# Optimization experiments

Hardware: AMD Instinct MI355X
Metric: run time of the kernel (lower is better)

## Reference

```python
import jax, jax.numpy as jnp
import numpy as np

DIM = 384; KEY_DIM = 32; HEADS = 8; ATTN_RATIO = 4; RES = 14
D = ATTN_RATIO * KEY_DIM          # 128
DH = D * HEADS                    # 1024
QK = HEADS * KEY_DIM              # 256
B = 64
EPS = 1e-5
SCALE = KEY_DIM ** -0.5


def _bn(x, p):
    # inference-mode BatchNorm; p = [gamma, beta, mean, var] each [C]; channel axis = 1
    g, b, m, v = p
    shp = (1, -1) + (1,) * (x.ndim - 2)
    return (x - m.reshape(shp)) * jax.lax.rsqrt(v.reshape(shp) + EPS) * g.reshape(shp) + b.reshape(shp)


def _bn_params(k, c):
    k1, k2, k3, k4 = jax.random.split(k, 4)
    gamma = 1.0 + 0.1 * jax.random.normal(k1, (c,), dtype=jnp.float32)
    beta = 0.02 * jax.random.normal(k2, (c,), dtype=jnp.float32)
    mean = 0.1 * jax.random.normal(k3, (c,), dtype=jnp.float32)
    var = jax.random.uniform(k4, (c,), dtype=jnp.float32) + 0.5
    return jnp.stack([gamma, beta, mean, var])


def setup_inputs() -> dict:
    key = jax.random.key(0)
    ks = jax.random.split(key, 24)
    def rn(i, shape, s=0.05):
        return s * jax.random.normal(ks[i], shape, dtype=jnp.float32)
    # relative-position bias index table: offset (|dy|,|dx|) -> dy*RES+dx
    coords = np.stack(np.meshgrid(np.arange(RES), np.arange(RES), indexing='ij'), -1).reshape(-1, 2)
    off = np.abs(coords[:, None, :] - coords[None, :, :])  # [N,N,2]
    bias_idxs = jnp.asarray(off[..., 0] * RES + off[..., 1], dtype=jnp.int32)  # [N,N]
    return {
        'x': jax.random.normal(ks[0], (B, DIM, RES, RES), dtype=jnp.float32),
        'wq': rn(1, (QK, DIM)), 'bq': rn(2, (QK,)), 'bnq': _bn_params(ks[3], QK),
        'wk': rn(4, (QK, DIM)), 'bk': rn(5, (QK,)), 'bnk': _bn_params(ks[6], QK),
        'wv': rn(7, (DH, DIM)), 'bv': rn(8, (DH,)), 'bnv': _bn_params(ks[9], DH),
        'wvl': rn(10, (DH, 1, 3, 3)), 'bvl': rn(11, (DH,)), 'bnvl': _bn_params(ks[12], DH),
        'th1w': rn(13, (HEADS, HEADS), 0.2), 'th1b': rn(14, (HEADS,)),
        'th2w': rn(15, (HEADS, HEADS), 0.2), 'th2b': rn(16, (HEADS,)),
        'wp': rn(17, (DIM, DH)), 'bp': rn(18, (DIM,)), 'bnp': _bn_params(ks[19], DIM),
        'ab': rn(20, (HEADS, RES * RES), 0.1),
        'bias_idxs': bias_idxs,
    }


def reference(x, wq, bq, bnq, wk, bk, bnk, wv, bv, bnv, wvl, bvl, bnvl,
              th1w, th1b, th2w, th2b, wp, bp, bnp, ab, bias_idxs):
    Bn, C, H, W = x.shape
    N = H * W
    xf = x.reshape(Bn, C, N)
    # 1x1 conv + BN branches (channel GEMMs)
    q = _bn(jnp.einsum('oc,bcn->bon', wq, xf) + bq[None, :, None], bnq)
    k = _bn(jnp.einsum('oc,bcn->bon', wk, xf) + bk[None, :, None], bnk)
    v = _bn(jnp.einsum('oc,bcn->bon', wv, xf) + bv[None, :, None], bnv)  # [B,DH,N]
    # local value path: 3x3 depthwise conv + BN
    v_img = v.reshape(Bn, DH, H, W)
    v_local = jax.lax.conv_general_dilated(
        v_img, wvl, window_strides=(1, 1), padding='SAME',
        feature_group_count=DH, dimension_numbers=('NCHW', 'OIHW', 'NCHW'))
    v_local = _bn(v_local + bvl[None, :, None, None], bnvl)
    # attention
    qh = q.reshape(Bn, HEADS, KEY_DIM, N).transpose(0, 1, 3, 2)  # b h n d
    kh = k.reshape(Bn, HEADS, KEY_DIM, N)                        # b h d m
    vh = v.reshape(Bn, HEADS, D, N).transpose(0, 1, 3, 2)        # b h m e
    attn = jnp.einsum('bhnd,bhdm->bhnm', qh, kh) * SCALE
    attn = attn + ab[:, bias_idxs][None]                         # [1,H,N,N] positional bias
    attn = jnp.einsum('oh,bhnm->bonm', th1w, attn) + th1b[None, :, None, None]
    attn = jax.nn.softmax(attn, axis=-1)
    attn = jnp.einsum('oh,bhnm->bonm', th2w, attn) + th2b[None, :, None, None]
    out = jnp.einsum('bhnm,bhme->bhne', attn, vh)                # b h n e
    out = out.transpose(0, 1, 3, 2).reshape(Bn, DH, H, W) + v_local
    # proj: ReLU -> 1x1 conv -> BN
    out = jax.nn.relu(out)
    out = jnp.einsum('oc,bchw->bohw', wp, out) + bp[None, :, None, None]
    return _bn(out, bnp)
```

## Files before the change

kernel.cpp:

```cpp
#include <hip/hip_runtime.h>

#define B_     64
#define DIM_   384
#define RES_   14
#define N_     196
#define HEADS_ 8
#define KD_    32
#define D_     128
#define DH_    1024
#define QK_    256
#define CH_    1536
#define EPS_   1e-5f
#define SCALE_ 0.17677669529663687f

typedef unsigned short u16;
typedef unsigned int u32;
typedef short v8s __attribute__((ext_vector_type(8)));
typedef float v4f __attribute__((ext_vector_type(4)));
typedef u16  v4u __attribute__((ext_vector_type(4)));

static __device__ __forceinline__ u16 f2bf(float f) {
    unsigned int u = __builtin_bit_cast(unsigned int, f);
    u = (u + 0x7fffu + ((u >> 16) & 1u)) >> 16;
    return (u16)u;
}
static __device__ __forceinline__ float bf2f(u16 u) {
    unsigned int x = ((unsigned int)u) << 16;
    return __builtin_bit_cast(float, x);
}
static __device__ __forceinline__ u16 f2h(float f) {
    _Float16 h = (_Float16)f;
    return __builtin_bit_cast(u16, h);
}
static __device__ __forceinline__ float h2f(u16 u) {
    return (float)__builtin_bit_cast(_Float16, u);
}

#define WBI_OFF  0u
#define WPI_OFF  589824u
#define QI_OFF   983040u
#define KI_OFF   5177344u
#define VI_OFF   9371648u
#define PBI_OFF  24051712u
#define VLOC_U16 53411840u
#define TAIL_OFF 79101952u
#define TB_OFF   98770944u
#define ABT_OFF  98782720u
#define BIASE_OFF 98785920u

template<int KSTEPS>
static __device__ __forceinline__ void gemm_direct(
    const u16* __restrict__ Ag, const u16* __restrict__ Bg,
    v4f acc[4][4], int tid)
{
    const int lane = tid & 63, w = tid >> 6;
    const int wm = (w & 1) * 64, wn = (w >> 1) * 64;
    const int quad = lane >> 4, l16 = lane & 15;
    const u16* pa = Ag + quad * 1024 + (wm + l16) * 8;
    const u16* pb = Bg + quad * 1024 + (wn + l16) * 8;
    v8s a[2][4], b[2][4];
    #pragma unroll
    for (int i = 0; i < 4; i++) {
        a[0][i] = *(const v8s*)(pa + i * 128);
        b[0][i] = *(const v8s*)(pb + i * 128);
    }
    #pragma unroll
    for (int ks = 0; ks < KSTEPS; ks++) {
        const int cur = ks & 1, nxt = cur ^ 1;
        if (ks + 1 < KSTEPS) {
            const u16* qa = pa + (size_t)(ks + 1) * 4096;
            const u16* qb = pb + (size_t)(ks + 1) * 4096;
            #pragma unroll
            for (int i = 0; i < 4; i++) {
                a[nxt][i] = *(const v8s*)(qa + i * 128);
                b[nxt][i] = *(const v8s*)(qb + i * 128);
            }
        }
        #pragma unroll
        for (int i = 0; i < 4; i++)
            #pragma unroll
            for (int j = 0; j < 4; j++)
                acc[i][j] = __builtin_amdgcn_mfma_f32_16x16x32_bf16(a[cur][i], b[cur][j], acc[i][j], 0, 0, 0);
    }
}

__global__ __launch_bounds__(256) void k_castW(
    const float* __restrict__ wq, const float* __restrict__ wk,
    const float* __restrict__ wv, const float* __restrict__ wp,
    const float* __restrict__ ab,
    const float* __restrict__ th1w, const float* __restrict__ th1b,
    const float* __restrict__ bq, const float* __restrict__ bnq,
    const float* __restrict__ bk, const float* __restrict__ bnk,
    const float* __restrict__ bv, const float* __restrict__ bnv,
    const float* __restrict__ bp, const float* __restrict__ bnp,
    const float* __restrict__ bvl, const float* __restrict__ bnvl,
    u16* __restrict__ WbI, u16* __restrict__ WpI,
    float* __restrict__ abT1, float* __restrict__ TB)
{
    int i = blockIdx.x * 256 + threadIdx.x;
    if (i < 589824) {
        int mt = i / 49152, rem = i % 49152;
        int ks = rem >> 12, r2 = rem & 4095;
        int q = r2 >> 10, row = (r2 >> 3) & 127, e = r2 & 7;
        int c = mt * 128 + row, k = ks * 32 + q * 8 + e;
        float v = (c < 256) ? wq[c * 384 + k]
                : (c < 512) ? wk[(c - 256) * 384 + k]
                            : wv[(size_t)(c - 512) * 384 + k];
        WbI[i] = f2bf(v);
    } else if (i < 983040) {
        int j = i - 589824;
        int mt = j >> 17, rem = j & 131071;
        int ks = rem >> 12, r2 = rem & 4095;
        int q = r2 >> 10, row = (r2 >> 3) & 127, e = r2 & 7;
        int p = mt * 128 + row, k = ks * 32 + q * 8 + e;
        WpI[j] = f2bf(wp[(size_t)p * 1024 + k]);
    } else if (i < 984608) {
        int j = i - 983040;
        int idx = j >> 3, o = j & 7;
        float a = th1b[o];
        #pragma unroll
        for (int h = 0; h < 8; h++) a += th1w[o * 8 + h] * ab[h * N_ + idx];
        abT1[j] = a;
    } else if (i < 987552) {
        int j = i - 984608;
        if (j < 256) {
            int c = j;
            float s = bnq[c] * rsqrtf(bnq[768 + c] + EPS_);
            float t = (bq[c] - bnq[512 + c]) * s + bnq[256 + c];
            TB[c] = s * SCALE_; TB[256 + c] = t * SCALE_;
        } else if (j < 512) {
            int c = j - 256;
            float s = bnk[c] * rsqrtf(bnk[768 + c] + EPS_);
            float t = (bk[c] - bnk[512 + c]) * s + bnk[256 + c];
            TB[512 + c] = s; TB[768 + c] = t;
        } else if (j < 1536) {
            int c = j - 512;
            float s = bnv[c] * rsqrtf(bnv[3072 + c] + EPS_);
            float t = (bv[c] - bnv[2048 + c]) * s + bnv[1024 + c];
            TB[1024 + c] = s; TB[2048 + c] = t;
        } else if (j < 1920) {
            int c = j - 1536;
            float s = bnp[c] * rsqrtf(bnp[1152 + c] + EPS_);
            float t = (bp[c] - bnp[768 + c]) * s + bnp[384 + c];
            TB[3072 + c] = s; TB[3456 + c] = t;
        } else {
            int c = j - 1920;
            float s = bnvl[c] * rsqrtf(bnvl[3072 + c] + EPS_);
            float t = (bvl[c] - bnvl[2048 + c]) * s + bnvl[1024 + c];
            TB[3840 + c] = s; TB[4864 + c] = t;
        }
    }
}

__global__ __launch_bounds__(256) void k_bias(
    const float* __restrict__ abT1, const int* __restrict__ bidx,
    float* __restrict__ biasE)
{
    int i = blockIdx.x * 256 + threadIdx.x;
    if (i >= N_ * 8 * N_) return;
    int m = i % N_;
    int t = i / N_;
    int o = t & 7;
    int n = t >> 3;
    biasE[i] = abT1[bidx[n * N_ + m] * 8 + o] - 5.f;
}

__global__ __launch_bounds__(256) void k_castX(
    const float* __restrict__ x, u16* __restrict__ xI)
{
    __shared__ float T[64][65];
    const int tid = threadIdx.x;
    const int n0 = blockIdx.x * 64;
    const int k0 = blockIdx.y * 64;
    const int b  = blockIdx.z;
    const int c = tid & 63, r4 = tid >> 6;
    #pragma unroll
    for (int i = 0; i < 16; i++) {
        int kr = i * 4 + r4;
        int gn = n0 + c;
        T[kr][c] = (gn < N_) ? x[((size_t)b * DIM_ + k0 + kr) * N_ + gn] : 0.f;
    }
    __syncthreads();
    #pragma unroll
    for (int it = 0; it < 16; it++) {
        int j = it * 256 + tid;
        int kk = j & 63, nn = j >> 6;
        int k = k0 + kk, n = n0 + nn;
        xI[(size_t)b * 98304 + (n >> 7) * 49152 + (k >> 5) * 4096
           + ((k >> 3) & 3) * 1024 + (n & 127) * 8 + (k & 7)] = f2bf(T[kk][nn]);
    }
}

__global__ __launch_bounds__(256) void k_qkv(
    const u16* __restrict__ WbI, const u16* __restrict__ xI,
    const float* __restrict__ TB,
    u16* __restrict__ qI, u16* __restrict__ kI, u16* __restrict__ vI)
{
    const int tid = threadIdx.x;
    const int L = blockIdx.x + 2 * (blockIdx.y + 12 * blockIdx.z);
    const int idx = L >> 3;
    const int b  = (L & 7) * 8 + idx / 24;
    const int r  = idx % 24;
    const int mt = r >> 1, nt = r & 1;
    v4f acc[4][4] = {};
    gemm_direct<12>(WbI + (size_t)mt * 49152,
                    xI + ((size_t)b * 2 + nt) * 49152, acc, tid);

    const int lane = tid & 63, w = tid >> 6;
    const int wm = (w & 1) * 64, wn = (w >> 1) * 64;
    const int quad = lane >> 4, l16 = lane & 15;
    #pragma unroll
    for (int i = 0; i < 4; i++) {
        #pragma unroll
        for (int j = 0; j < 4; j++) {
            int gc = mt * 128 + wm + i * 16 + quad * 4;
            int n  = nt * 128 + wn + j * 16 + l16;
            v4f v = acc[i][j];
            if (gc < 256) {
                v4f s = *(const v4f*)&TB[gc];
                v4f t = *(const v4f*)&TB[256 + gc];
                v4u u;
                #pragma unroll
                for (int r2 = 0; r2 < 4; r2++) u[r2] = f2bf(v[r2] * s[r2] + t[r2]);
                *(v4u*)&qI[((size_t)(b * 8 + (gc >> 5)) * 256 + n) * 32 + (gc & 31)] = u;
            } else if (gc < 512) {
                int c = gc - 256;
                v4f s = *(const v4f*)&TB[512 + c];
                v4f t = *(const v4f*)&TB[768 + c];
                v4u u;
                #pragma unroll
                for (int r2 = 0; r2 < 4; r2++) u[r2] = f2bf(v[r2] * s[r2] + t[r2]);
                *(v4u*)&kI[((size_t)(b * 8 + (c >> 5)) * 256 + n) * 32 + (c & 31)] = u;
            } else {
                int c = gc - 512;
                if (n < 224) {
                    int o = c >> 7, e = c & 127;
                    u16* base = vI + ((size_t)(b * 8 + o) * 7 + (n >> 5)) * 4096
                                + ((n >> 3) & 3) * 1024 + (n & 7);
                    #pragma unroll
                    for (int r2 = 0; r2 < 4; r2++) {
                        u16 outv = 0;
                        if (n < N_) outv = f2bf(v[r2] * TB[1024 + c + r2] + TB[2048 + c + r2]);
                        base[(e + r2) * 8] = outv;
                    }
                }
            }
        }
    }
}

__global__ __launch_bounds__(256) void k_dwconv(
    const u16* __restrict__ vI, const float* __restrict__ wvl,
    const float* __restrict__ TB, u16* __restrict__ vlocI)
{
    __shared__ u16 V[64 * 230];
    const int tid = threadIdx.x;
    const int sub = blockIdx.x;
    const int b   = blockIdx.y;
    const int o   = sub >> 1;
    const int e0  = (sub & 1) * 64;
    const u16* img = vI + (size_t)(b * 8 + o) * 28672;

    {
        const int quad = tid >> 6, l = tid & 63;
        #pragma unroll
        for (int i = 0; i < 7; i++) {
            v8s u = *(const v8s*)&img[i * 4096 + quad * 1024 + (e0 + l) * 8];
            const u32* ui = (const u32*)&u;
            int m0 = i * 32 + quad * 8;
            u32* dst = (u32*)&V[l * 230 + m0];
            #pragma unroll
            for (int c = 0; c < 4; c++) dst[c] = ui[c];
        }
    }
    __syncthreads();

    const int e = tid & 63, j = tid >> 6;
    const int cg = sub * 64 + e;
    const int y0 = j * 4;
    const int ny = (j == 3) ? 2 : 4;
    float wgt[9];
    #pragma unroll
    for (int k = 0; k < 9; k++) wgt[k] = wvl[cg * 9 + k];
    const float sc = TB[3840 + cg], sh = TB[4864 + cg];
    u32 po[4][7];

    for (int yi = 0; yi < ny; yi++) {
        int y = y0 + yi;
        float a[3][16];
        #pragma unroll
        for (int dy = 0; dy < 3; dy++) {
            int yy = y + dy - 1;
            a[dy][0] = 0.f; a[dy][15] = 0.f;
            if (yy < 0 || yy > 13) {
                #pragma unroll
                for (int x = 1; x < 15; x++) a[dy][x] = 0.f;
            } else {
                const u16* rp = &V[e * 230 + yy * 14];
                #pragma unroll
                for (int c4 = 0; c4 < 7; c4++) {
                    u32 u = *(const u32*)&rp[c4 * 2];
                    a[dy][1 + 2 * c4] = bf2f((u16)(u & 0xffffu));
                    a[dy][2 + 2 * c4] = bf2f((u16)(u >> 16));
                }
            }
        }
        #pragma unroll
        for (int xp = 0; xp < 7; xp++) {
            u32 pk = 0;
            #pragma unroll
            for (int half = 0; half < 2; half++) {
                int x = 2 * xp + half;
                float s = 0.f;
                #pragma unroll
                for (int dy = 0; dy < 3; dy++)
                    #pragma unroll
                    for (int kx = 0; kx < 3; kx++)
                        s += wgt[dy * 3 + kx] * a[dy][x + kx];
                u16 bv = f2bf(s * sc + sh);
                pk |= ((u32)bv) << (16 * half);
            }
            po[yi][xp] = pk;
        }
    }
    __syncthreads();

    for (int yi = 0; yi < ny; yi++) {
        u32* dst = (u32*)&V[e * 196 + (y0 + yi) * 14];
        #pragma unroll
        for (int xp = 0; xp < 7; xp++) dst[xp] = po[yi][xp];
    }
    __syncthreads();

    for (int it = 0; it < 7; it++) {
        int idx = it * 256 + tid;
        if (idx < 1568) {
            int g = idx / 196, n = idx - g * 196;
            v4u lo, hi;
            #pragma unroll
            for (int r = 0; r < 4; r++) lo[r] = V[(g * 8 + r) * 196 + n];
            #pragma unroll
            for (int r = 0; r < 4; r++) hi[r] = V[(g * 8 + 4 + r) * 196 + n];
            u16* dst = vlocI + ((size_t)(b * 2 + (n >> 7)) * 32 + sub * 2 + (g >> 2)) * 4096
                     + (g & 3) * 1024 + (n & 127) * 8;
            *(v4u*)dst = lo;
            *(v4u*)(dst + 4) = hi;
        }
    }
}

__global__ __launch_bounds__(256) void k_attn_av(
    const u16* __restrict__ qI, const u16* __restrict__ kI,
    const u16* __restrict__ vI,
    const float* __restrict__ th1w,
    const float* __restrict__ th2w, const float* __restrict__ th2b,
    const float* __restrict__ biasE,
    const u16* __restrict__ vlocI, u16* __restrict__ aoI)
{
    __shared__ u16 Sl[8 * 8 * 228];
    __shared__ float red[64][4];
    __shared__ float invS[64];
    const int tid = threadIdx.x;
    const int w = tid >> 6, lane = tid & 63;
    const int quad = lane >> 4, l16 = lane & 15;
    const int L = blockIdx.x + 25 * blockIdx.y;
    const int idx = L >> 3;
    const int b  = (L & 7) * 8 + idx / 25;
    const int qt = idx % 25;
    const int n0 = qt * 8;

    #pragma unroll
    for (int hh = 0; hh < 2; hh++) {
        int h = w * 2 + hh;
        const u16* qb = qI + (size_t)(b * 8 + h) * 8192;
        const u16* kb = kI + (size_t)(b * 8 + h) * 8192;
        v8s a = *(const v8s*)&qb[(n0 + l16) * 32 + quad * 8];
        #pragma unroll
        for (int mt = 0; mt < 13; mt++) {
            v8s bfr = *(const v8s*)&kb[(mt * 16 + l16) * 32 + quad * 8];
            v4f acc = {};
            acc = __builtin_amdgcn_mfma_f32_16x16x32_bf16(a, bfr, acc, 0, 0, 0);
            if (quad < 2) {
                #pragma unroll
                for (int r = 0; r < 4; r++) {
                    int q = quad * 4 + r;
                    Sl[(h * 8 + q) * 228 + mt * 16 + l16] = f2h(acc[r]);
                }
            }
        }
    }
    __syncthreads();

    const int m = tid;
    const bool mact = (m < N_);
    for (int q = 0; q < 8; q++) {
        int n = n0 + q;
        if (mact && n < N_) {
            const float* bE = biasE + (size_t)n * 1568 + m;
            float S[8];
            #pragma unroll
            for (int h = 0; h < 8; h++) S[h] = h2f(Sl[(h * 8 + q) * 228 + m]);
            float E[8];
            #pragma unroll
            for (int o = 0; o < 8; o++) {
                float a = bE[o * 196];
                #pragma unroll
                for (int h = 0; h < 8; h++) a += th1w[o * 8 + h] * S[h];
                E[o] = __expf(a);
            }
            #pragma unroll
            for (int o = 0; o < 8; o++)
                Sl[(o * 8 + q) * 228 + m] = f2h(E[o]);
        }
    }
    __syncthreads();

    {
        int r = tid >> 2, quarter = tid & 3;
        int mstart = quarter * 48;
        int cnt = (quarter == 3) ? 26 : 24;
        const u16* rowp = &Sl[r * 228 + mstart];
        float s = 0.f;
        for (int i = 0; i < cnt; i++) {
            u32 u = *(const u32*)&rowp[i * 2];
            s += h2f((u16)(u & 0xffffu)) + h2f((u16)(u >> 16));
        }
        red[r][quarter] = s;
    }
    __syncthreads();
    if (tid < 64)
        invS[tid] = 1.f / (red[tid][0] + red[tid][1] + red[tid][2] + red[tid][3]);
    __syncthreads();

    for (int q = 0; q < 8; q++) {
        bool valid = mact && (n0 + q < N_);
        float p[8];
        if (valid) {
            float sc[8];
            #pragma unroll
            for (int h = 0; h < 8; h++)
                sc[h] = h2f(Sl[(h * 8 + q) * 228 + m]) * invS[h * 8 + q];
            #pragma unroll
            for (int o = 0; o < 8; o++) {
                float v = th2b[o];
                #pragma unroll
                for (int h = 0; h < 8; h++) v += th2w[o * 8 + h] * sc[h];
                p[o] = v;
            }
        }
        if (m < 224) {
            #pragma unroll
            for (int o = 0; o < 8; o++)
                Sl[(o * 8 + q) * 228 + m] = valid ? f2bf(p[o]) : (u16)0;
        }
    }
    __syncthreads();

    {
        const int half_ = n0 >> 7;
        const int row0 = n0 & 127;
        const int n = n0 + l16;
        const bool act = (l16 < 8) && (n < N_);
        for (int oo = 0; oo < 2; oo++) {
            const int o = w * 2 + oo;
            const u16* vb = vI + (size_t)(b * 8 + o) * 28672;
            const u16* prow = &Sl[(o * 8 + (l16 & 7)) * 228];
            #pragma unroll
            for (int eh = 0; eh < 2; eh++) {
                v4f acc[4] = {};
                v8s a[2][4];
                const u16* ab0 = vb + quad * 1024 + (eh * 64 + l16) * 8;
                #pragma unroll
                for (int e = 0; e < 4; e++) a[0][e] = *(const v8s*)(ab0 + e * 128);
                #pragma unroll
                for (int ks = 0; ks < 7; ks++) {
                    const int cur = ks & 1, nxt = cur ^ 1;
                    if (ks < 6) {
                        const u16* an = ab0 + (size_t)(ks + 1) * 4096;
                        #pragma unroll
                        for (int e = 0; e < 4; e++) a[nxt][e] = *(const v8s*)(an + e * 128);
                    }
                    v8s bfr = *(const v8s*)&prow[ks * 32 + quad * 8];
                    #pragma unroll
                    for (int e = 0; e < 4; e++)
                        acc[e] = __builtin_amdgcn_mfma_f32_16x16x32_bf16(a[cur][e], bfr, acc[e], 0, 0, 0);
                }
                if (act) {
                    #pragma unroll
                    for (int e = 0; e < 4; e++) {
                        const int c0 = o * 128 + (eh * 4 + e) * 16 + quad * 4;
                        const size_t ioff = ((size_t)(b * 2 + half_) * 32 + (c0 >> 5)) * 4096
                                          + ((c0 >> 3) & 3) * 1024 + (size_t)(row0 + l16) * 8 + (c0 & 7);
                        v4u lv = *(const v4u*)&vlocI[ioff];
                        v4u u;
                        #pragma unroll
                        for (int r = 0; r < 4; r++)
                            u[r] = f2bf(fmaxf(acc[e][r] + bf2f(lv[r]), 0.f));
                        *(v4u*)&aoI[ioff] = u;
                    }
                }
            }
        }
    }
}

__global__ __launch_bounds__(256) void k_proj(
    const u16* __restrict__ WpI, const u16* __restrict__ aoI,
    const float* __restrict__ TB, float* __restrict__ out)
{
    const int tid = threadIdx.x;
    const int L = blockIdx.x + 2 * (blockIdx.y + 3 * blockIdx.z);
    const int idx = L >> 3;
    const int b  = (L & 7) * 8 + idx / 6;
    const int r  = idx % 6;
    const int mt = r >> 1, nt = r & 1;
    v4f acc[4][4] = {};
    gemm_direct<32>(WpI + (size_t)mt * 131072,
                    aoI + ((size_t)b * 2 + nt) * 131072, acc, tid);

    const int lane = tid & 63, w = tid >> 6;
    const int wm = (w & 1) * 64, wn = (w >> 1) * 64;
    const int quad = lane >> 4, l16 = lane & 15;
    #pragma unroll
    for (int i = 0; i < 4; i++) {
        #pragma unroll
        for (int j = 0; j < 4; j++) {
            int p0 = mt * 128 + wm + i * 16 + quad * 4;
            int n  = nt * 128 + wn + j * 16 + l16;
            if (n < N_) {
                v4f s = *(const v4f*)&TB[3072 + p0];
                v4f t = *(const v4f*)&TB[3456 + p0];
                #pragma unroll
                for (int r2 = 0; r2 < 4; r2++)
                    out[((size_t)b * DIM_ + p0 + r2) * N_ + n] = acc[i][j][r2] * s[r2] + t[r2];
            }
        }
    }
}

extern "C" void kernel_launch(void* const* d_in, const int* in_sizes, int n_in,
                              void* d_out, int out_size, void* d_ws, size_t ws_size,
                              hipStream_t stream)
{
    const float* x    = (const float*)d_in[0];
    const float* wq   = (const float*)d_in[1];
    const float* bq   = (const float*)d_in[2];
    const float* bnq  = (const float*)d_in[3];
    const float* wk   = (const float*)d_in[4];
    const float* bk   = (const float*)d_in[5];
    const float* bnk  = (const float*)d_in[6];
    const float* wv   = (const float*)d_in[7];
    const float* bv   = (const float*)d_in[8];
    const float* bnv  = (const float*)d_in[9];
    const float* wvl  = (const float*)d_in[10];
    const float* bvl  = (const float*)d_in[11];
    const float* bnvl = (const float*)d_in[12];
    const float* th1w = (const float*)d_in[13];
    const float* th1b = (const float*)d_in[14];
    const float* th2w = (const float*)d_in[15];
    const float* th2b = (const float*)d_in[16];
    const float* wp   = (const float*)d_in[17];
    const float* bp   = (const float*)d_in[18];
    const float* bnp  = (const float*)d_in[19];
    const float* ab   = (const float*)d_in[20];
    const int*   bidx = (const int*)d_in[21];
    float* out = (float*)d_out;

    u16* wsb  = (u16*)d_ws;
    u16* WbI  = wsb + WBI_OFF;
    u16* WpI  = wsb + WPI_OFF;
    u16* qI   = wsb + QI_OFF;
    u16* kI   = wsb + KI_OFF;
    u16* vI   = wsb + VI_OFF;
    u16* vlocI = wsb + VLOC_U16;
    u16* xI   = wsb + TAIL_OFF;
    u16* aoI  = wsb + TAIL_OFF;
    float* TB    = (float*)(wsb + TB_OFF);
    float* abT1  = (float*)(wsb + ABT_OFF);
    float* biasE = (float*)(wsb + BIASE_OFF);

    k_castW<<<dim3(3859), 256, 0, stream>>>(wq, wk, wv, wp, ab, th1w, th1b,
                                            bq, bnq, bk, bnk, bv, bnv, bp, bnp, bvl, bnvl,
                                            WbI, WpI, abT1, TB);
    k_bias<<<dim3((N_ * 8 * N_ + 255) / 256), 256, 0, stream>>>(abT1, bidx, biasE);
    k_castX<<<dim3(4, 6, B_), 256, 0, stream>>>(x, xI);
    k_qkv<<<dim3(2, 12, B_), 256, 0, stream>>>(WbI, xI, TB, qI, kI, vI);
    k_dwconv<<<dim3(16, B_), 256, 0, stream>>>(vI, wvl, TB, vlocI);
    k_attn_av<<<dim3(25, B_), 256, 0, stream>>>(qI, kI, vI, th1w, th2w, th2b,
                                                biasE, vlocI, aoI);
    k_proj<<<dim3(2, 3, B_), 256, 0, stream>>>(WpI, aoI, TB, out);
}
```

Baseline: 283.2 us.

## Widen attention kernel to 512 threads, one wave per head

The attention+AV kernel goes from 256 to 512 threads per block. Each of the 8 waves now owns one head for the QK^T and AV MFMA phases, and the softmax and talking-heads phases split the 8 query rows across two thread halves. The row-sum reduction is spread over 8 partials per row instead of 4. The aim is more parallelism per block and shorter per-thread serial work, at the cost of higher per-block register and thread demand, which may reduce how many blocks fit on a CU.

```diff
diff --git a/kernel.cpp b/kernel.cpp
--- a/kernel.cpp
+++ b/kernel.cpp
@@ -41,7 +41,6 @@
 #define QI_OFF   983040u
 #define KI_OFF   5177344u
 #define VI_OFF   9371648u
-#define PBI_OFF  24051712u
 #define VLOC_U16 53411840u
 #define TAIL_OFF 79101952u
 #define TB_OFF   98770944u
@@ -349,7 +348,7 @@
     }
 }
 
-__global__ __launch_bounds__(256) void k_attn_av(
+__global__ __launch_bounds__(512) void k_attn_av(
     const u16* __restrict__ qI, const u16* __restrict__ kI,
     const u16* __restrict__ vI,
     const float* __restrict__ th1w,
@@ -358,7 +357,7 @@
     const u16* __restrict__ vlocI, u16* __restrict__ aoI)
 {
     __shared__ u16 Sl[8 * 8 * 228];
-    __shared__ float red[64][4];
+    __shared__ float red[64][8];
     __shared__ float invS[64];
     const int tid = threadIdx.x;
     const int w = tid >> 6, lane = tid & 63;
@@ -369,9 +368,8 @@
     const int qt = idx % 25;
     const int n0 = qt * 8;
 
-    #pragma unroll
-    for (int hh = 0; hh < 2; hh++) {
-        int h = w * 2 + hh;
+    {
+        const int h = w;
         const u16* qb = qI + (size_t)(b * 8 + h) * 8192;
         const u16* kb = kI + (size_t)(b * 8 + h) * 8192;
         v8s a = *(const v8s*)&qb[(n0 + l16) * 32 + quad * 8];
@@ -391,9 +389,11 @@
     }
     __syncthreads();
 
-    const int m = tid;
+    const int m = tid & 255;
+    const int qh = tid >> 8;
     const bool mact = (m < N_);
-    for (int q = 0; q < 8; q++) {
+    for (int qq = 0; qq < 4; qq++) {
+        int q = qh * 4 + qq;
         int n = n0 + q;
         if (mact && n < N_) {
             const float* bE = biasE + (size_t)n * 1568 + m;
@@ -416,23 +416,28 @@
     __syncthreads();
 
     {
-        int r = tid >> 2, quarter = tid & 3;
-        int mstart = quarter * 48;
-        int cnt = (quarter == 3) ? 26 : 24;
+        int r = tid >> 3, oct = tid & 7;
+        int mstart = oct * 24;
+        int cnt = (oct == 7) ? 14 : 12;
         const u16* rowp = &Sl[r * 228 + mstart];
         float s = 0.f;
         for (int i = 0; i < cnt; i++) {
             u32 u = *(const u32*)&rowp[i * 2];
             s += h2f((u16)(u & 0xffffu)) + h2f((u16)(u >> 16));
         }
-        red[r][quarter] = s;
-    }
-    __syncthreads();
-    if (tid < 64)
-        invS[tid] = 1.f / (red[tid][0] + red[tid][1] + red[tid][2] + red[tid][3]);
-    __syncthreads();
-
-    for (int q = 0; q < 8; q++) {
+        red[r][oct] = s;
+    }
+    __syncthreads();
+    if (tid < 64) {
+        float s = 0.f;
+        #pragma unroll
+        for (int i = 0; i < 8; i++) s += red[tid][i];
+        invS[tid] = 1.f / s;
+    }
+    __syncthreads();
+
+    for (int qq = 0; qq < 4; qq++) {
+        int q = qh * 4 + qq;
         bool valid = mact && (n0 + q < N_);
         float p[8];
         if (valid) {
@@ -461,43 +466,41 @@
         const int row0 = n0 & 127;
         const int n = n0 + l16;
         const bool act = (l16 < 8) && (n < N_);
-        for (int oo = 0; oo < 2; oo++) {
-            const int o = w * 2 + oo;
-            const u16* vb = vI + (size_t)(b * 8 + o) * 28672;
-            const u16* prow = &Sl[(o * 8 + (l16 & 7)) * 228];
-            #pragma unroll
-            for (int eh = 0; eh < 2; eh++) {
-                v4f acc[4] = {};
-                v8s a[2][4];
-                const u16* ab0 = vb + quad * 1024 + (eh * 64 + l16) * 8;
-                #pragma unroll
-                for (int e = 0; e < 4; e++) a[0][e] = *(const v8s*)(ab0 + e * 128);
-                #pragma unroll
-                for (int ks = 0; ks < 7; ks++) {
-                    const int cur = ks & 1, nxt = cur ^ 1;
-                    if (ks < 6) {
-                        const u16* an = ab0 + (size_t)(ks + 1) * 4096;
-                        #pragma unroll
-                        for (int e = 0; e < 4; e++) a[nxt][e] = *(const v8s*)(an + e * 128);
-                    }
-                    v8s bfr = *(const v8s*)&prow[ks * 32 + quad * 8];
+        const int o = w;
+        const u16* vb = vI + (size_t)(b * 8 + o) * 28672;
+        const u16* prow = &Sl[(o * 8 + (l16 & 7)) * 228];
+        #pragma unroll
+        for (int eh = 0; eh < 2; eh++) {
+            v4f acc[4] = {};
+            v8s a[2][4];
+            const u16* ab0 = vb + quad * 1024 + (eh * 64 + l16) * 8;
+            #pragma unroll
+            for (int e = 0; e < 4; e++) a[0][e] = *(const v8s*)(ab0 + e * 128);
+            #pragma unroll
+            for (int ks = 0; ks < 7; ks++) {
+                const int cur = ks & 1, nxt = cur ^ 1;
+                if (ks < 6) {
+                    const u16* an = ab0 + (size_t)(ks + 1) * 4096;
                     #pragma unroll
-                    for (int e = 0; e < 4; e++)
-                        acc[e] = __builtin_amdgcn_mfma_f32_16x16x32_bf16(a[cur][e], bfr, acc[e], 0, 0, 0);
+                    for (int e = 0; e < 4; e++) a[nxt][e] = *(const v8s*)(an + e * 128);
                 }
-                if (act) {
+                v8s bfr = *(const v8s*)&prow[ks * 32 + quad * 8];
+                #pragma unroll
+                for (int e = 0; e < 4; e++)
+                    acc[e] = __builtin_amdgcn_mfma_f32_16x16x32_bf16(a[cur][e], bfr, acc[e], 0, 0, 0);
+            }
+            if (act) {
+                #pragma unroll
+                for (int e = 0; e < 4; e++) {
+                    const int c0 = o * 128 + (eh * 4 + e) * 16 + quad * 4;
+                    const size_t ioff = ((size_t)(b * 2 + half_) * 32 + (c0 >> 5)) * 4096
+                                      + ((c0 >> 3) & 3) * 1024 + (size_t)(row0 + l16) * 8 + (c0 & 7);
+                    v4u lv = *(const v4u*)&vlocI[ioff];
+                    v4u u;
                     #pragma unroll
-                    for (int e = 0; e < 4; e++) {
-                        const int c0 = o * 128 + (eh * 4 + e) * 16 + quad * 4;
-                        const size_t ioff = ((size_t)(b * 2 + half_) * 32 + (c0 >> 5)) * 4096
-                                          + ((c0 >> 3) & 3) * 1024 + (size_t)(row0 + l16) * 8 + (c0 & 7);
-                        v4u lv = *(const v4u*)&vlocI[ioff];
-                        v4u u;
-                        #pragma unroll
-                        for (int r = 0; r < 4; r++)
-                            u[r] = f2bf(fmaxf(acc[e][r] + bf2f(lv[r]), 0.f));
-                        *(v4u*)&aoI[ioff] = u;
-                    }
+                    for (int r = 0; r < 4; r++)
+                        u[r] = f2bf(fmaxf(acc[e][r] + bf2f(lv[r]), 0.f));
+                    *(v4u*)&aoI[ioff] = u;
                 }
             }
         }
@@ -586,7 +589,7 @@
     k_castX<<<dim3(4, 6, B_), 256, 0, stream>>>(x, xI);
     k_qkv<<<dim3(2, 12, B_), 256, 0, stream>>>(WbI, xI, TB, qI, kI, vI);
     k_dwconv<<<dim3(16, B_), 256, 0, stream>>>(vI, wvl, TB, vlocI);
-    k_attn_av<<<dim3(25, B_), 256, 0, stream>>>(qI, kI, vI, th1w, th2w, th2b,
+    k_attn_av<<<dim3(25, B_), 512, 0, stream>>>(qI, kI, vI, th1w, th2w, th2b,
                                                 biasE, vlocI, aoI);
     k_proj<<<dim3(2, 3, B_), 256, 0, stream>>>(WpI, aoI, TB, out);
 }
```

Result: faster. 270.1 us (-4.6%).
